# Performance work log

Hardware: AMD Instinct MI355X
Metric: run time of the kernel (lower is better)

The kernel has to match this reference:

```python
import jax, jax.numpy as jnp
import numpy as np

B = 65536

def setup_inputs() -> dict:
    key = jax.random.key(0)
    ks = jax.random.split(key, 8)
    x = jax.random.normal(ks[0], (B, 784), dtype=jnp.float32)
    conv_w = jnp.ones((3, 3), dtype=jnp.float32)  # Parameter(ones((3,3)))
    # Linear layers (stored as [in, out] so forward is x @ W + b)
    w1 = jax.random.normal(ks[1], (676, 100), dtype=jnp.float32) * 0.04
    b1 = jnp.zeros((100,), dtype=jnp.float32)
    w2 = jax.random.normal(ks[2], (100, 10), dtype=jnp.float32) * 0.1
    b2 = jnp.zeros((10,), dtype=jnp.float32)
    w3 = jax.random.normal(ks[3], (10, 10), dtype=jnp.float32) * 0.3
    b3 = jnp.zeros((10,), dtype=jnp.float32)
    return {"x": x, "conv_w": conv_w, "w1": w1, "b1": b1,
            "w2": w2, "b2": b2, "w3": w3, "b3": b3}


def _convolve_batch(x, conv_w):
    # x: [B, 28, 28]; valid 3x3 correlation (tensordot of patch with weight, no flip)
    lhs = x[:, None, :, :]                 # [B, 1, 28, 28] NCHW
    rhs = conv_w[None, None, :, :]         # [1, 1, 3, 3] OIHW
    out = jax.lax.conv_general_dilated(
        lhs, rhs, window_strides=(1, 1), padding="VALID",
        dimension_numbers=("NCHW", "OIHW", "NCHW"))
    return out[:, 0]                       # [B, 26, 26]


def reference(x, conv_w, w1, b1, w2, b2, w3, b3):
    b = x.shape[0]
    h = _convolve_batch(x.reshape(b, 28, 28), conv_w)   # [B, 26, 26]
    h = h.reshape(b, 676)
    h = jax.nn.relu(h @ w1 + b1)
    h = jax.nn.relu(h @ w2 + b2)
    return h @ w3 + b3                                   # [B, 10]
```

## Files before the change

### kernel.cpp

```cpp
#include <hip/hip_runtime.h>
#include <hip/hip_bf16.h>

#define K1 784
#define N1 100
#define KT 25
#define NTT 7
#define NTP 8

typedef __attribute__((ext_vector_type(8))) short bf16x8;
typedef __attribute__((ext_vector_type(4))) float f32x4;

__device__ __forceinline__ ushort f2bf(float f) {
    union { float f; unsigned u; } v; v.f = f;
    unsigned u = v.u;
    return (ushort)((u + 0x7FFFu + ((u >> 16) & 1u)) >> 16);
}

__device__ __forceinline__ bf16x8 pack_bf16x8(float4 a, float4 b) {
    union { unsigned u[4]; bf16x8 v; } r;
    asm("v_cvt_pk_bf16_f32 %0, %1, %2" : "=v"(r.u[0]) : "v"(a.x), "v"(a.y));
    asm("v_cvt_pk_bf16_f32 %0, %1, %2" : "=v"(r.u[1]) : "v"(a.z), "v"(a.w));
    asm("v_cvt_pk_bf16_f32 %0, %1, %2" : "=v"(r.u[2]) : "v"(b.x), "v"(b.y));
    asm("v_cvt_pk_bf16_f32 %0, %1, %2" : "=v"(r.u[3]) : "v"(b.z), "v"(b.w));
    return r.v;
}

__device__ __forceinline__ void gload_lds16(const void* g, void* l) {
    __builtin_amdgcn_global_load_lds(
        (const __attribute__((address_space(1))) void*)g,
        (__attribute__((address_space(3))) void*)l, 16, 0, 0);
}

__global__ void build_wp(const float* __restrict__ w1,
                         const float* __restrict__ conv_w,
                         ushort* __restrict__ wp) {
    int idx = blockIdx.x * blockDim.x + threadIdx.x;
    if (idx >= KT * NTP * 512) return;
    int j = idx & 7, lane = (idx >> 3) & 63, rest = idx >> 9;
    int nt = rest & 7, kt = rest >> 3;
    int k = kt * 32 + (lane >> 4) * 8 + j;
    int n = nt * 16 + (lane & 15);
    float w = 0.f;
    if (k < K1 && n < N1) {
        int py = k / 28, px = k % 28;
        #pragma unroll
        for (int dy = 0; dy < 3; ++dy) {
            int oy = py - dy; if (oy < 0 || oy > 25) continue;
            #pragma unroll
            for (int dx = 0; dx < 3; ++dx) {
                int ox = px - dx; if (ox < 0 || ox > 25) continue;
                w += conv_w[dy * 3 + dx] * w1[(oy * 26 + ox) * N1 + n];
            }
        }
    }
    wp[(size_t)(kt * NTP + nt) * 512 + lane * 8 + j] = f2bf(w);
}

__global__ __launch_bounds__(256, 4) void fused_mfma(
    const float* __restrict__ x, const ushort* __restrict__ wp,
    const float* __restrict__ b1, const float* __restrict__ w2,
    const float* __restrict__ b2, const float* __restrict__ w3,
    const float* __restrict__ b3, float* __restrict__ out)
{
    __shared__ __attribute__((aligned(16))) ushort bsm[2][NTP * 512];
    __shared__ float w2t[10][112];
    __shared__ float w3s[100];
    __shared__ float b1s[100];
    __shared__ float b2s[10], b3s[10];

    const int tid  = threadIdx.x;
    const int lane = tid & 63;
    const int lo16 = lane & 15, hi4 = lane >> 4;
    const size_t row0 = (size_t)blockIdx.x * 64 + (tid >> 6) * 16;

    for (int e = tid; e < 10 * 112; e += 256) w2t[e / 112][e % 112] = 0.f;
    __syncthreads();
    for (int e = tid; e < 1000; e += 256) w2t[e % 10][e / 10] = w2[e];
    for (int e = tid; e < 100; e += 256) { w3s[e] = w3[e]; b1s[e] = b1[e]; }
    if (tid < 10) { b2s[tid] = b2[tid]; b3s[tid] = b3[tid]; }
    __syncthreads();

    const float* xr = x + (row0 + lo16) * K1;

    f32x4 acc[NTT];
    #pragma unroll
    for (int n = 0; n < NTT; ++n) { f32x4 z = {0.f,0.f,0.f,0.f}; acc[n] = z; }

    {
        const ushort* src = wp + tid * 8;
        gload_lds16(src,        &bsm[0][tid * 8]);
        gload_lds16(src + 2048, &bsm[0][tid * 8 + 2048]);
    }
    __builtin_amdgcn_sched_barrier(0);
    float4 cur0 = *reinterpret_cast<const float4*>(xr + hi4 * 8);
    float4 cur1 = *reinterpret_cast<const float4*>(xr + hi4 * 8 + 4);
    float4 nxt0 = cur0, nxt1 = cur1;
    asm volatile("s_waitcnt vmcnt(2)" ::: "memory");
    __builtin_amdgcn_s_barrier();
    asm volatile("" ::: "memory");

    for (int kt = 0; kt < KT; ++kt) {
        const int cur = kt & 1;
        if (kt < KT - 1) {
            const ushort* src = wp + (size_t)(kt + 1) * (NTP * 512) + tid * 8;
            gload_lds16(src,        &bsm[cur ^ 1][tid * 8]);
            gload_lds16(src + 2048, &bsm[cur ^ 1][tid * 8 + 2048]);
            __builtin_amdgcn_sched_barrier(0);
            int nb = (kt + 1) * 32 + hi4 * 8;
            if (nb > K1 - 8) nb = K1 - 8;
            nxt0 = *reinterpret_cast<const float4*>(xr + nb);
            nxt1 = *reinterpret_cast<const float4*>(xr + nb + 4);
        }
        bf16x8 ah = pack_bf16x8(cur0, cur1);
        const ushort* bb = &bsm[cur][lane * 8];
        #pragma unroll
        for (int nt = 0; nt < NTT; ++nt) {
            bf16x8 bh = *reinterpret_cast<const bf16x8*>(bb + nt * 512);
            acc[nt] = __builtin_amdgcn_mfma_f32_16x16x32_bf16(ah, bh,
                                                              acc[nt], 0,0,0);
        }
        asm volatile("s_waitcnt vmcnt(2) lgkmcnt(0)" ::: "memory");
        __builtin_amdgcn_s_barrier();
        asm volatile("" ::: "memory");
        cur0 = nxt0; cur1 = nxt1;
    }

    __syncthreads();

    float h1v[NTT][4];
    #pragma unroll
    for (int nt = 0; nt < NTT; ++nt) {
        int col = nt * 16 + lo16;
        bool valid = col < N1;
        float bb = valid ? b1s[valid ? col : 0] : 0.f;
        #pragma unroll
        for (int r = 0; r < 4; ++r)
            h1v[nt][r] = valid ? fmaxf(acc[nt][r] + bb, 0.f) : 0.f;
    }

    const int jj = lo16;
    float o[4] = {0.f, 0.f, 0.f, 0.f};
    #pragma unroll
    for (int j = 0; j < 10; ++j) {
        float pj[4] = {0.f, 0.f, 0.f, 0.f};
        #pragma unroll
        for (int nt = 0; nt < NTT; ++nt) {
            float wv = w2t[j][nt * 16 + lo16];
            #pragma unroll
            for (int r = 0; r < 4; ++r) pj[r] += h1v[nt][r] * wv;
        }
        #pragma unroll
        for (int mask = 8; mask >= 1; mask >>= 1)
            #pragma unroll
            for (int r = 0; r < 4; ++r)
                pj[r] += __shfl_xor(pj[r], mask, 16);
        float w3v = (jj < 10) ? w3s[j * 10 + jj] : 0.f;
        #pragma unroll
        for (int r = 0; r < 4; ++r) {
            float h2 = fmaxf(pj[r] + b2s[j], 0.f);
            o[r] += h2 * w3v;
        }
    }

    if (jj < 10) {
        #pragma unroll
        for (int r = 0; r < 4; ++r)
            out[(row0 + hi4 * 4 + r) * 10 + jj] = o[r] + b3s[jj];
    }
}

extern "C" void kernel_launch(void* const* d_in, const int* in_sizes, int n_in,
                              void* d_out, int out_size, void* d_ws, size_t ws_size,
                              hipStream_t stream) {
    const float* x     = (const float*)d_in[0];
    const float* convw = (const float*)d_in[1];
    const float* w1    = (const float*)d_in[2];
    const float* b1    = (const float*)d_in[3];
    const float* w2    = (const float*)d_in[4];
    const float* b2    = (const float*)d_in[5];
    const float* w3    = (const float*)d_in[6];
    const float* b3    = (const float*)d_in[7];
    float* out  = (float*)d_out;
    ushort* wp  = (ushort*)d_ws;

    build_wp<<<(KT * NTP * 512 + 255) / 256, 256, 0, stream>>>(w1, convw, wp);
    fused_mfma<<<65536 / 64, 256, 0, stream>>>(x, wp, b1, w2, b2, w3, b3, out);
}
```

Before: 53.44 us.

## Compute two row tiles per wave with triple-buffered weights and deeper x prefetch

Each wave now handles 32 rows instead of 16, so every B-fragment read from LDS feeds two MFMAs and the weight tile traffic per row is halved. The weight staging moves from double to triple buffering, x loads are prefetched three K-steps ahead in a 4-slot register ring, and the K loop is fully unrolled with hand-tuned vmcnt waits. The grid is halved and occupancy is lowered to 2 blocks per SIMD group to make room for the larger register footprint. The cost is more VGPRs and fewer resident waves, which leaves less latency hiding through occupancy on what is a bandwidth-bound read of x.

```diff
diff --git a/kernel.cpp b/kernel.cpp
--- a/kernel.cpp
+++ b/kernel.cpp
@@ -56,13 +56,13 @@
     wp[(size_t)(kt * NTP + nt) * 512 + lane * 8 + j] = f2bf(w);
 }
 
-__global__ __launch_bounds__(256, 4) void fused_mfma(
+__global__ __launch_bounds__(256, 2) void fused_mfma(
     const float* __restrict__ x, const ushort* __restrict__ wp,
     const float* __restrict__ b1, const float* __restrict__ w2,
     const float* __restrict__ b2, const float* __restrict__ w3,
     const float* __restrict__ b3, float* __restrict__ out)
 {
-    __shared__ __attribute__((aligned(16))) ushort bsm[2][NTP * 512];
+    __shared__ __attribute__((aligned(16))) ushort bsm[3][NTP * 512];
     __shared__ float w2t[10][112];
     __shared__ float w3s[100];
     __shared__ float b1s[100];
@@ -71,7 +71,8 @@
     const int tid  = threadIdx.x;
     const int lane = tid & 63;
     const int lo16 = lane & 15, hi4 = lane >> 4;
-    const size_t row0 = (size_t)blockIdx.x * 64 + (tid >> 6) * 16;
+    const int wid  = tid >> 6;
+    const size_t rowbase = (size_t)blockIdx.x * 128 + wid * 32;
 
     for (int e = tid; e < 10 * 112; e += 256) w2t[e / 112][e % 112] = 0.f;
     __syncthreads();
@@ -80,92 +81,124 @@
     if (tid < 10) { b2s[tid] = b2[tid]; b3s[tid] = b3[tid]; }
     __syncthreads();
 
-    const float* xr = x + (row0 + lo16) * K1;
-
-    f32x4 acc[NTT];
-    #pragma unroll
-    for (int n = 0; n < NTT; ++n) { f32x4 z = {0.f,0.f,0.f,0.f}; acc[n] = z; }
-
-    {
-        const ushort* src = wp + tid * 8;
-        gload_lds16(src,        &bsm[0][tid * 8]);
-        gload_lds16(src + 2048, &bsm[0][tid * 8 + 2048]);
-    }
+    const float* xr0 = x + (rowbase + lo16) * K1;
+    const float* xr1 = xr0 + (size_t)16 * K1;
+
+    f32x4 acc[2][NTT];
+    #pragma unroll
+    for (int m = 0; m < 2; ++m)
+        #pragma unroll
+        for (int n = 0; n < NTT; ++n) { f32x4 z = {0.f,0.f,0.f,0.f}; acc[m][n] = z; }
+
+    float4 xs[4][4];
+
+#define STAGE(KTB)                                                            \
+    { const ushort* src = wp + (size_t)(KTB) * (NTP * 512) + tid * 8;         \
+      ushort* dst = &bsm[(KTB) % 3][tid * 8];                                 \
+      gload_lds16(src, dst); gload_lds16(src + 2048, dst + 2048); }
+#define LOADX(KTL, SLOT)                                                      \
+    { int nb = (KTL) * 32 + hi4 * 8;                                          \
+      if (nb > K1 - 8) nb = K1 - 8;               \
+      xs[SLOT][0] = *reinterpret_cast<const float4*>(xr0 + nb);               \
+      xs[SLOT][1] = *reinterpret_cast<const float4*>(xr0 + nb + 4);           \
+      xs[SLOT][2] = *reinterpret_cast<const float4*>(xr1 + nb);               \
+      xs[SLOT][3] = *reinterpret_cast<const float4*>(xr1 + nb + 4); }
+
+    STAGE(0);
     __builtin_amdgcn_sched_barrier(0);
-    float4 cur0 = *reinterpret_cast<const float4*>(xr + hi4 * 8);
-    float4 cur1 = *reinterpret_cast<const float4*>(xr + hi4 * 8 + 4);
-    float4 nxt0 = cur0, nxt1 = cur1;
-    asm volatile("s_waitcnt vmcnt(2)" ::: "memory");
+    LOADX(0, 0);
+    __builtin_amdgcn_sched_barrier(0);
+    STAGE(1);
+    __builtin_amdgcn_sched_barrier(0);
+    LOADX(1, 1);
+    LOADX(2, 2);
+    asm volatile("s_waitcnt vmcnt(14)" ::: "memory");
     __builtin_amdgcn_s_barrier();
     asm volatile("" ::: "memory");
 
+    #pragma unroll
     for (int kt = 0; kt < KT; ++kt) {
-        const int cur = kt & 1;
-        if (kt < KT - 1) {
-            const ushort* src = wp + (size_t)(kt + 1) * (NTP * 512) + tid * 8;
-            gload_lds16(src,        &bsm[cur ^ 1][tid * 8]);
-            gload_lds16(src + 2048, &bsm[cur ^ 1][tid * 8 + 2048]);
+        const int slot = kt % 4;
+        const int bslot = kt % 3;
+        if (kt <= KT - 3) {
+            STAGE(kt + 2);
             __builtin_amdgcn_sched_barrier(0);
-            int nb = (kt + 1) * 32 + hi4 * 8;
-            if (nb > K1 - 8) nb = K1 - 8;
-            nxt0 = *reinterpret_cast<const float4*>(xr + nb);
-            nxt1 = *reinterpret_cast<const float4*>(xr + nb + 4);
-        }
-        bf16x8 ah = pack_bf16x8(cur0, cur1);
-        const ushort* bb = &bsm[cur][lane * 8];
+        }
+        if (kt <= KT - 4) {
+            LOADX(kt + 3, (kt + 3) % 4);
+        }
+        bf16x8 ah0 = pack_bf16x8(xs[slot][0], xs[slot][1]);
+        bf16x8 ah1 = pack_bf16x8(xs[slot][2], xs[slot][3]);
+        const ushort* bb = &bsm[bslot][lane * 8];
         #pragma unroll
         for (int nt = 0; nt < NTT; ++nt) {
             bf16x8 bh = *reinterpret_cast<const bf16x8*>(bb + nt * 512);
-            acc[nt] = __builtin_amdgcn_mfma_f32_16x16x32_bf16(ah, bh,
-                                                              acc[nt], 0,0,0);
-        }
-        asm volatile("s_waitcnt vmcnt(2) lgkmcnt(0)" ::: "memory");
-        __builtin_amdgcn_s_barrier();
-        asm volatile("" ::: "memory");
-        cur0 = nxt0; cur1 = nxt1;
+            acc[0][nt] = __builtin_amdgcn_mfma_f32_16x16x32_bf16(ah0, bh,
+                                                          acc[0][nt], 0,0,0);
+            acc[1][nt] = __builtin_amdgcn_mfma_f32_16x16x32_bf16(ah1, bh,
+                                                          acc[1][nt], 0,0,0);
+        }
+        if (kt < KT - 1) {
+            if (kt == 0)
+                asm volatile("s_waitcnt vmcnt(14) lgkmcnt(0)" ::: "memory");
+            else if (kt <= KT - 4)
+                asm volatile("s_waitcnt vmcnt(10) lgkmcnt(0)" ::: "memory");
+            else if (kt == KT - 3)
+                asm volatile("s_waitcnt vmcnt(6) lgkmcnt(0)" ::: "memory");
+            else
+                asm volatile("s_waitcnt vmcnt(0) lgkmcnt(0)" ::: "memory");
+            __builtin_amdgcn_s_barrier();
+            asm volatile("" ::: "memory");
+        }
     }
+#undef STAGE
+#undef LOADX
 
     __syncthreads();
 
-    float h1v[NTT][4];
-    #pragma unroll
-    for (int nt = 0; nt < NTT; ++nt) {
-        int col = nt * 16 + lo16;
-        bool valid = col < N1;
-        float bb = valid ? b1s[valid ? col : 0] : 0.f;
-        #pragma unroll
-        for (int r = 0; r < 4; ++r)
-            h1v[nt][r] = valid ? fmaxf(acc[nt][r] + bb, 0.f) : 0.f;
-    }
+    float h1v[2][NTT][4];
+    #pragma unroll
+    for (int m = 0; m < 2; ++m)
+        #pragma unroll
+        for (int nt = 0; nt < NTT; ++nt) {
+            int col = nt * 16 + lo16;
+            bool valid = col < N1;
+            float bb = valid ? b1s[valid ? col : 0] : 0.f;
+            #pragma unroll
+            for (int r = 0; r < 4; ++r)
+                h1v[m][nt][r] = valid ? fmaxf(acc[m][nt][r] + bb, 0.f) : 0.f;
+        }
 
     const int jj = lo16;
-    float o[4] = {0.f, 0.f, 0.f, 0.f};
-    #pragma unroll
-    for (int j = 0; j < 10; ++j) {
-        float pj[4] = {0.f, 0.f, 0.f, 0.f};
-        #pragma unroll
-        for (int nt = 0; nt < NTT; ++nt) {
-            float wv = w2t[j][nt * 16 + lo16];
-            #pragma unroll
-            for (int r = 0; r < 4; ++r) pj[r] += h1v[nt][r] * wv;
-        }
-        #pragma unroll
-        for (int mask = 8; mask >= 1; mask >>= 1)
+    #pragma unroll
+    for (int m = 0; m < 2; ++m) {
+        float o[4] = {0.f, 0.f, 0.f, 0.f};
+        #pragma unroll
+        for (int j = 0; j < 10; ++j) {
+            float pj[4] = {0.f, 0.f, 0.f, 0.f};
+            #pragma unroll
+            for (int nt = 0; nt < NTT; ++nt) {
+                float wv = w2t[j][nt * 16 + lo16];
+                #pragma unroll
+                for (int r = 0; r < 4; ++r) pj[r] += h1v[m][nt][r] * wv;
+            }
+            #pragma unroll
+            for (int mask = 8; mask >= 1; mask >>= 1)
+                #pragma unroll
+                for (int r = 0; r < 4; ++r)
+                    pj[r] += __shfl_xor(pj[r], mask, 16);
+            float w3v = (jj < 10) ? w3s[j * 10 + jj] : 0.f;
+            #pragma unroll
+            for (int r = 0; r < 4; ++r) {
+                float h2 = fmaxf(pj[r] + b2s[j], 0.f);
+                o[r] += h2 * w3v;
+            }
+        }
+        if (jj < 10) {
             #pragma unroll
             for (int r = 0; r < 4; ++r)
-                pj[r] += __shfl_xor(pj[r], mask, 16);
-        float w3v = (jj < 10) ? w3s[j * 10 + jj] : 0.f;
-        #pragma unroll
-        for (int r = 0; r < 4; ++r) {
-            float h2 = fmaxf(pj[r] + b2s[j], 0.f);
-            o[r] += h2 * w3v;
-        }
-    }
-
-    if (jj < 10) {
-        #pragma unroll
-        for (int r = 0; r < 4; ++r)
-            out[(row0 + hi4 * 4 + r) * 10 + jj] = o[r] + b3s[jj];
+                out[(rowbase + m * 16 + hi4 * 4 + r) * 10 + jj] = o[r] + b3s[jj];
+        }
     }
 }
 
@@ -184,5 +217,5 @@
     ushort* wp  = (ushort*)d_ws;
 
     build_wp<<<(KT * NTP * 512 + 255) / 256, 256, 0, stream>>>(w1, convw, wp);
-    fused_mfma<<<65536 / 64, 256, 0, stream>>>(x, wp, b1, w2, b2, w3, b3, out);
-}
+    fused_mfma<<<65536 / 128, 256, 0, stream>>>(x, wp, b1, w2, b2, w3, b3, out);
+}
```

After: 51.54 us (median of 2 runs). -3.6%, faster.
